# Kernel tuning notes

Measured on AMD Instinct MI355X. Metric: run time of the kernel, lower is better.

## Reference

```python
import jax, jax.numpy as jnp
import numpy as np

LOG2 = float(np.log(2.0))

def _ssp(x):
    # shifted softplus: ln(0.5*(exp(x)+1)) = softplus(x) - ln 2
    return jax.nn.softplus(x) - LOG2

def setup_inputs() -> dict:
    key = jax.random.key(0)
    ks = jax.random.split(key, 8)
    B, N, D = 32, 512, 1024
    H = D // 2
    s = lambda fan_in: 1.0 / np.sqrt(fan_in)
    return {
        "representation": jax.random.normal(ks[0], (B, N, D), jnp.float32),
        "R": jax.random.normal(ks[1], (B, N, 3), jnp.float32),
        "atom_mask": jnp.ones((B, N), jnp.float32),
        "W1": jax.random.normal(ks[2], (D, H), jnp.float32) * s(D),
        "b1": jnp.zeros((H,), jnp.float32),
        "W2": jax.random.normal(ks[3], (H, 1), jnp.float32) * s(H),
        "b2": jnp.zeros((1,), jnp.float32),
        "Wc1": jax.random.normal(ks[4], (D, H), jnp.float32) * s(D),
        "bc1": jnp.zeros((H,), jnp.float32),
        "Wc2": jax.random.normal(ks[5], (H, 1), jnp.float32) * s(H),
        "bc2": jnp.zeros((1,), jnp.float32),
    }

def reference(representation, R, atom_mask, W1, b1, W2, b2, Wc1, bc1, Wc2, bc2):
    B, N, _ = representation.shape
    # Atomwise pyramidal MLP: n_in -> n_in//2 (shifted softplus) -> 1
    yi = _ssp(jnp.einsum("bnd,dh->bnh", representation, W1) + b1)
    yi = jnp.einsum("bnh,ho->bno", yi, W2) + b2            # [B,N,1]
    # masked sum pool over atoms (mean=0, stddev=1 so standardize is identity)
    y = jnp.sum(yi * atom_mask[..., None], axis=1)          # [B,1]

    # pairwise distances with safe sqrt (diag is exactly zero)
    diff = R[:, None, :, :] - R[:, :, None, :]              # [B,N,N,3]
    d2 = jnp.sum(diff * diff, axis=-1)                      # [B,N,N]
    dist = jnp.where(d2 > 0, jnp.sqrt(jnp.where(d2 > 0, d2, 1.0)), 0.0)

    eye = jnp.eye(N, dtype=dist.dtype)
    tot_mask = atom_mask[:, None, :] * atom_mask[:, :, None] * (1.0 - eye)
    keep = (tot_mask != 0).astype(dist.dtype)               # [B,N,N]
    dist = dist * keep

    # charge net: Dense(n_in, n_in//2, ssp) -> Dense(n_in//2, 1)
    q = _ssp(jnp.einsum("bnd,dh->bnh", representation, Wc1) + bc1)
    q = jnp.einsum("bnh,ho->bno", q, Wc2) + bc2             # [B,N,1]

    inv2 = (1e-5 + dist) ** -2                              # [B,N,N]
    coulomb = q[:, :, 0][:, None, :] * inv2 * q             # [B,N,N] (q_j * inv * q_i)
    coulomb = coulomb * keep
    e = jnp.sum(coulomb, axis=(1, 2))                       # [B]

    return y + e[:, None]                                   # [B,1]
```

## Files before the change

kernel.cpp:

```cpp
#include <hip/hip_runtime.h>
#include <math.h>


typedef unsigned short u16;
typedef unsigned int u32;
typedef __bf16 bf16x8 __attribute__((ext_vector_type(8)));
typedef float f32x4 __attribute__((ext_vector_type(4)));

#define GK 1024

#define GLOAD_LDS16(g, l) __builtin_amdgcn_global_load_lds( \
    (const __attribute__((address_space(1))) void*)(g),     \
    (__attribute__((address_space(3))) void*)(l), 16, 0, 0)

__device__ __forceinline__ u16 f2bf(float f) {
    u32 u = __float_as_uint(f);
    return (u16)((u + 0x7FFFu + ((u >> 16) & 1u)) >> 16);
}

__device__ __forceinline__ float ssp_f(float x) {
    return __logf(0.5f * (__expf(x) + 1.0f));
}

__device__ __forceinline__ float ssp_slow(float x) {
    return fmaxf(x, 0.0f) + log1pf(expf(-fabsf(x))) - 0.6931471805599453f;
}


__global__ __launch_bounds__(256) void conv_a(const float* __restrict__ in,
                                              u16* __restrict__ out) {
    int i = (blockIdx.x * 256 + threadIdx.x) * 8;
    float4 x = *(const float4*)(in + i);
    float4 y = *(const float4*)(in + i + 4);
    union { u16 h[8]; uint4 v; } o;
    o.h[0] = f2bf(x.x); o.h[1] = f2bf(x.y); o.h[2] = f2bf(x.z); o.h[3] = f2bf(x.w);
    o.h[4] = f2bf(y.x); o.h[5] = f2bf(y.y); o.h[6] = f2bf(y.z); o.h[7] = f2bf(y.w);
    *(uint4*)(out + i) = o.v;
}

__global__ __launch_bounds__(256) void conv_w(const float* __restrict__ W1,
                                              const float* __restrict__ Wc1,
                                              u16* __restrict__ Bt) {
    __shared__ float tile[32][33];
    const int k0 = blockIdx.x * 32;
    const int n0 = blockIdx.y * 32;
    const float* src = (n0 < 512) ? W1 : Wc1;
    const int ns0 = (n0 < 512) ? n0 : n0 - 512;
    const int t = threadIdx.x;
#pragma unroll
    for (int j = 0; j < 4; j++) {
        int idx = j * 256 + t;
        int kl = idx >> 5, nl = idx & 31;
        tile[kl][nl] = src[(size_t)(k0 + kl) * 512 + ns0 + nl];
    }
    __syncthreads();
#pragma unroll
    for (int j = 0; j < 4; j++) {
        int idx = j * 256 + t;
        int nl = idx >> 5, kl = idx & 31;
        Bt[(size_t)(n0 + nl) * 1024 + k0 + kl] = f2bf(tile[kl][nl]);
    }
}


__global__ __launch_bounds__(256) void gemm_mfma(
    const u16* __restrict__ A,
    const u16* __restrict__ Bt,
    const float* __restrict__ b1, const float* __restrict__ W2,
    const float* __restrict__ bc1, const float* __restrict__ Wc2,
    float* __restrict__ yi_part, float* __restrict__ q_part)
{
    __shared__ u16 As[128 * 32];
    __shared__ u16 Bs[128 * 32];
    const int bm = blockIdx.x;
    const int bn = blockIdx.y;
    const int tid = threadIdx.x;
    const int w = tid >> 6, lane = tid & 63;
    const int wave_m = w & 1, wave_n = w >> 1;
    const int lm = lane & 15, q = lane >> 4;

    f32x4 acc[4][4];
#pragma unroll
    for (int i = 0; i < 4; i++)
#pragma unroll
        for (int j = 0; j < 4; j++)
            acc[i][j] = (f32x4){0.0f, 0.0f, 0.0f, 0.0f};

    const size_t a_base = (size_t)(bm * 128) * GK;
    const size_t b_base = (size_t)(bn * 128) * GK;

    int goff[2];
#pragma unroll
    for (int p = 0; p < 2; p++) {
        int c = (w * 2 + p) * 64 + lane;
        int row = c >> 2;
        int slot = c & 3;
        int k8 = slot ^ ((row >> 2) & 3);
        goff[p] = row * GK + k8 * 8;
    }

    int aoff[4], boff[4];
#pragma unroll
    for (int i = 0; i < 4; i++) {
        int mrow = wave_m * 64 + i * 16 + lm;
        aoff[i] = mrow * 32 + (q ^ ((mrow >> 2) & 3)) * 8;
        int nrow = wave_n * 64 + i * 16 + lm;
        boff[i] = nrow * 32 + (q ^ ((nrow >> 2) & 3)) * 8;
    }

    for (int kt = 0; kt < GK; kt += 32) {
#pragma unroll
        for (int p = 0; p < 2; p++) {
            GLOAD_LDS16(A + a_base + kt + goff[p], &As[(w * 2 + p) << 9]);
            GLOAD_LDS16(Bt + b_base + kt + goff[p], &Bs[(w * 2 + p) << 9]);
        }
        __syncthreads();
        bf16x8 af[4], bfr[4];
#pragma unroll
        for (int i = 0; i < 4; i++) {
            af[i] = *(const bf16x8*)&As[aoff[i]];
            bfr[i] = *(const bf16x8*)&Bs[boff[i]];
        }
#pragma unroll
        for (int i = 0; i < 4; i++)
#pragma unroll
            for (int j = 0; j < 4; j++)
                acc[i][j] = __builtin_amdgcn_mfma_f32_16x16x32_bf16(af[i], bfr[j],
                                                                    acc[i][j], 0, 0, 0);
        __syncthreads();
    }

    const bool is_q = (bn >= 4);
    const float* bb = is_q ? bc1 : b1;
    const float* vv = is_q ? Wc2 : W2;
    float* target = is_q ? q_part : yi_part;
    const int cb0 = (bn & 3) * 128 + wave_n * 64;
    float bias[4], v[4];
#pragma unroll
    for (int j = 0; j < 4; j++) {
        int c = cb0 + j * 16 + lm;
        bias[j] = bb[c];
        v[j] = vv[c];
    }
    const int rowg0 = bm * 128 + wave_m * 64;
#pragma unroll
    for (int i = 0; i < 4; i++) {
#pragma unroll
        for (int r = 0; r < 4; r++) {
            float s = 0.0f;
#pragma unroll
            for (int j = 0; j < 4; j++)
                s += v[j] * ssp_f(acc[i][j][r] + bias[j]);
            s += __shfl_xor(s, 1);
            s += __shfl_xor(s, 2);
            s += __shfl_xor(s, 4);
            s += __shfl_xor(s, 8);
            if (lm == 0) atomicAdd(&target[rowg0 + i * 16 + q * 4 + r], s);
        }
    }
}


__global__ __launch_bounds__(256) void coulomb_k(
    const float* __restrict__ R, const float* __restrict__ mask,
    const float* __restrict__ yi_part, const float* __restrict__ q_part,
    const float* __restrict__ b2p, const float* __restrict__ bc2p,
    float* __restrict__ out)
{
    const int N = 512;
    const int b = blockIdx.y;
    const int chunk = blockIdx.x;
    __shared__ float Rx[512], Ry[512], Rz[512], QM[512];
    __shared__ float rbuf[4];
    const int tid = threadIdx.x;
    const float bc2 = bc2p[0];
    const float b2 = b2p[0];

    for (int j = tid; j < N; j += 256) {
        float m = mask[b * N + j];
        const float* rp = R + ((size_t)b * N + j) * 3;
        Rx[j] = rp[0];
        Ry[j] = rp[1];
        Rz[j] = rp[2];
        QM[j] = (q_part[b * N + j] + bc2) * m;
    }
    __syncthreads();

    const int i = chunk * 64 + (tid & 63);
    const int js = (tid >> 6) * 128;
    const float xi = Rx[i], yi = Ry[i], zi = Rz[i], qmi = QM[i];
    float e = 0.0f;
    for (int j = js; j < js + 128; j++) {
        float dx = xi - Rx[j];
        float dy = yi - Ry[j];
        float dz = zi - Rz[j];
        float d2 = dx * dx + dy * dy + dz * dz;
        float dist = sqrtf(d2);
        float t = 1e-5f + dist;
        float term = qmi * QM[j] / (t * t);
        e += (j == i) ? 0.0f : term;
    }
    if (tid < 64) {
        int ii = chunk * 64 + tid;
        e += (yi_part[b * N + ii] + b2) * mask[b * N + ii];
    }
    for (int off = 32; off > 0; off >>= 1) e += __shfl_down(e, off, 64);
    if ((tid & 63) == 0) rbuf[tid >> 6] = e;
    __syncthreads();
    if (tid == 0) atomicAdd(&out[b], rbuf[0] + rbuf[1] + rbuf[2] + rbuf[3]);
}


#define BM 128
#define BN 64
#define BK 16

__global__ __launch_bounds__(256) void mlp_gemm(
    const float* __restrict__ A, const float* __restrict__ W1,
    const float* __restrict__ Wc1, const float* __restrict__ b1,
    const float* __restrict__ bc1, const float* __restrict__ W2,
    const float* __restrict__ Wc2, float* __restrict__ yi_part,
    float* __restrict__ q_part)
{
    const int K = 1024;
    const int bm = blockIdx.x;
    const int bn = blockIdx.y;
    const bool is_q = (bn >= 8);
    const float* __restrict__ W = is_q ? Wc1 : W1;
    const int j0 = (bn & 7) * BN;

    __shared__ float As[BK][BM + 4];
    __shared__ float Bs[BK][BN + 4];
    __shared__ float red[BM];

    const int tid = threadIdx.x;
    const int tx = tid & 15;
    const int ty = tid >> 4;

    float acc[8][4];
#pragma unroll
    for (int r = 0; r < 8; r++)
#pragma unroll
        for (int c = 0; c < 4; c++) acc[r][c] = 0.0f;

    const int a_row = tid >> 2;
    const int a_k4 = (tid & 3) * 4;
    const float* Arow0 = A + (size_t)(bm * BM + a_row) * K;
    const float* Arow1 = Arow0 + (size_t)64 * K;
    const int w_k = tid >> 4;
    const int w_j = (tid & 15) * 4;

    for (int kt = 0; kt < K; kt += BK) {
        float4 av0 = *(const float4*)(Arow0 + kt + a_k4);
        float4 av1 = *(const float4*)(Arow1 + kt + a_k4);
        float4 wv = *(const float4*)(W + (size_t)(kt + w_k) * 512 + j0 + w_j);
        __syncthreads();
        As[a_k4 + 0][a_row] = av0.x;
        As[a_k4 + 1][a_row] = av0.y;
        As[a_k4 + 2][a_row] = av0.z;
        As[a_k4 + 3][a_row] = av0.w;
        As[a_k4 + 0][a_row + 64] = av1.x;
        As[a_k4 + 1][a_row + 64] = av1.y;
        As[a_k4 + 2][a_row + 64] = av1.z;
        As[a_k4 + 3][a_row + 64] = av1.w;
        *(float4*)&Bs[w_k][w_j] = wv;
        __syncthreads();
#pragma unroll
        for (int kk = 0; kk < BK; kk++) {
            float4 a0 = *(const float4*)&As[kk][ty * 8];
            float4 a1 = *(const float4*)&As[kk][ty * 8 + 4];
            float4 bv = *(const float4*)&Bs[kk][tx * 4];
            float ar[8] = {a0.x, a0.y, a0.z, a0.w, a1.x, a1.y, a1.z, a1.w};
            float bc[4] = {bv.x, bv.y, bv.z, bv.w};
#pragma unroll
            for (int r = 0; r < 8; r++)
#pragma unroll
                for (int c = 0; c < 4; c++)
                    acc[r][c] = fmaf(ar[r], bc[c], acc[r][c]);
        }
    }

    const float* bb = is_q ? bc1 : b1;
    const float* vv = is_q ? Wc2 : W2;
    float bias[4], v[4];
#pragma unroll
    for (int c = 0; c < 4; c++) {
        bias[c] = bb[j0 + tx * 4 + c];
        v[c] = vv[j0 + tx * 4 + c];
    }
    if (tid < BM) red[tid] = 0.0f;
    __syncthreads();
#pragma unroll
    for (int r = 0; r < 8; r++) {
        float s = 0.0f;
#pragma unroll
        for (int c = 0; c < 4; c++)
            s += v[c] * ssp_slow(acc[r][c] + bias[c]);
        atomicAdd(&red[ty * 8 + r], s);
    }
    __syncthreads();
    float* target = is_q ? q_part : yi_part;
    if (tid < BM) atomicAdd(&target[(size_t)bm * BM + tid], red[tid]);
}


extern "C" void kernel_launch(void* const* d_in, const int* in_sizes, int n_in,
                              void* d_out, int out_size, void* d_ws, size_t ws_size,
                              hipStream_t stream) {
    const float* rep  = (const float*)d_in[0];
    const float* R    = (const float*)d_in[1];
    const float* mask = (const float*)d_in[2];
    const float* W1   = (const float*)d_in[3];
    const float* b1   = (const float*)d_in[4];
    const float* W2   = (const float*)d_in[5];
    const float* b2   = (const float*)d_in[6];
    const float* Wc1  = (const float*)d_in[7];
    const float* bc1  = (const float*)d_in[8];
    const float* Wc2  = (const float*)d_in[9];
    const float* bc2  = (const float*)d_in[10];
    float* out = (float*)d_out;

    const size_t szA = 16384ull * 1024 * 2;
    const size_t szB = 1024ull * 1024 * 2;
    const size_t need = szA + szB + 2 * 16384 * sizeof(float);

    if (ws_size >= need) {
        u16* Abf = (u16*)d_ws;
        u16* Btb = (u16*)((char*)d_ws + szA);
        float* yi_part = (float*)((char*)d_ws + szA + szB);
        float* q_part = yi_part + 16384;

        hipMemsetAsync(yi_part, 0, 2 * 16384 * sizeof(float), stream);
        hipMemsetAsync(d_out, 0, 32 * sizeof(float), stream);

        conv_a<<<8192, 256, 0, stream>>>(rep, Abf);
        conv_w<<<dim3(32, 32), 256, 0, stream>>>(W1, Wc1, Btb);
        gemm_mfma<<<dim3(128, 8), 256, 0, stream>>>(Abf, Btb, b1, W2, bc1, Wc2,
                                                    yi_part, q_part);
        coulomb_k<<<dim3(8, 32), 256, 0, stream>>>(R, mask, yi_part, q_part, b2, bc2, out);
    } else {
        float* yi_part = (float*)d_ws;
        float* q_part = yi_part + 16384;
        hipMemsetAsync(d_ws, 0, 2 * 16384 * sizeof(float), stream);
        hipMemsetAsync(d_out, 0, 32 * sizeof(float), stream);
        mlp_gemm<<<dim3(128, 16), 256, 0, stream>>>(rep, W1, Wc1, b1, bc1, W2, Wc2,
                                                    yi_part, q_part);
        coulomb_k<<<dim3(8, 32), 256, 0, stream>>>(R, mask, yi_part, q_part, b2, bc2, out);
    }
}
```

Measured before the change: 190.9 us.

## Merge conversion kernels, deepen GEMM K-tile, drop memsets and atomics

The two bf16 conversion kernels become one launch. The GEMM K step doubles from 32 to 64, with an 8-way XOR swizzle, and each block reduces its partial sums in shared memory before writing them to a per-column-block buffer with plain stores, so global atomics and both memsets go away. The Coulomb stage becomes one 1024-thread block per molecule that sums the partial buffers and writes the output directly. This cuts launch count and synchronisation, but the Coulomb stage now runs on only 32 blocks, which lowers its parallelism.

```diff
diff --git a/kernel.cpp b/kernel.cpp
--- a/kernel.cpp
+++ b/kernel.cpp
@@ -27,38 +27,41 @@
 }
 
 
-__global__ __launch_bounds__(256) void conv_a(const float* __restrict__ in,
-                                              u16* __restrict__ out) {
-    int i = (blockIdx.x * 256 + threadIdx.x) * 8;
-    float4 x = *(const float4*)(in + i);
-    float4 y = *(const float4*)(in + i + 4);
-    union { u16 h[8]; uint4 v; } o;
-    o.h[0] = f2bf(x.x); o.h[1] = f2bf(x.y); o.h[2] = f2bf(x.z); o.h[3] = f2bf(x.w);
-    o.h[4] = f2bf(y.x); o.h[5] = f2bf(y.y); o.h[6] = f2bf(y.z); o.h[7] = f2bf(y.w);
-    *(uint4*)(out + i) = o.v;
-}
-
-__global__ __launch_bounds__(256) void conv_w(const float* __restrict__ W1,
-                                              const float* __restrict__ Wc1,
-                                              u16* __restrict__ Bt) {
+__global__ __launch_bounds__(256) void prep(
+    const float* __restrict__ rep, const float* __restrict__ W1,
+    const float* __restrict__ Wc1, u16* __restrict__ Abf,
+    u16* __restrict__ Btb)
+{
     __shared__ float tile[32][33];
-    const int k0 = blockIdx.x * 32;
-    const int n0 = blockIdx.y * 32;
-    const float* src = (n0 < 512) ? W1 : Wc1;
-    const int ns0 = (n0 < 512) ? n0 : n0 - 512;
+    const int blk = blockIdx.x;
     const int t = threadIdx.x;
-#pragma unroll
-    for (int j = 0; j < 4; j++) {
-        int idx = j * 256 + t;
-        int kl = idx >> 5, nl = idx & 31;
-        tile[kl][nl] = src[(size_t)(k0 + kl) * 512 + ns0 + nl];
-    }
-    __syncthreads();
-#pragma unroll
-    for (int j = 0; j < 4; j++) {
-        int idx = j * 256 + t;
-        int nl = idx >> 5, kl = idx & 31;
-        Bt[(size_t)(n0 + nl) * 1024 + k0 + kl] = f2bf(tile[kl][nl]);
+    if (blk < 8192) {
+        int i = (blk * 256 + t) * 8;
+        float4 x = *(const float4*)(rep + i);
+        float4 y = *(const float4*)(rep + i + 4);
+        union { u16 h[8]; uint4 v; } o;
+        o.h[0] = f2bf(x.x); o.h[1] = f2bf(x.y); o.h[2] = f2bf(x.z); o.h[3] = f2bf(x.w);
+        o.h[4] = f2bf(y.x); o.h[5] = f2bf(y.y); o.h[6] = f2bf(y.z); o.h[7] = f2bf(y.w);
+        *(uint4*)(Abf + i) = o.v;
+    } else {
+        const int bb = blk - 8192;
+        const int k0 = (bb & 31) * 32;
+        const int n0 = (bb >> 5) * 32;
+        const float* src = (n0 < 512) ? W1 : Wc1;
+        const int ns0 = (n0 < 512) ? n0 : n0 - 512;
+#pragma unroll
+        for (int j = 0; j < 4; j++) {
+            int idx = j * 256 + t;
+            int kl = idx >> 5, nl = idx & 31;
+            tile[kl][nl] = src[(size_t)(k0 + kl) * 512 + ns0 + nl];
+        }
+        __syncthreads();
+#pragma unroll
+        for (int j = 0; j < 4; j++) {
+            int idx = j * 256 + t;
+            int nl = idx >> 5, kl = idx & 31;
+            Btb[(size_t)(n0 + nl) * 1024 + k0 + kl] = f2bf(tile[kl][nl]);
+        }
     }
 }
 
@@ -68,10 +71,11 @@
     const u16* __restrict__ Bt,
     const float* __restrict__ b1, const float* __restrict__ W2,
     const float* __restrict__ bc1, const float* __restrict__ Wc2,
-    float* __restrict__ yi_part, float* __restrict__ q_part)
+    float* __restrict__ parts)
 {
-    __shared__ u16 As[128 * 32];
-    __shared__ u16 Bs[128 * 32];
+    __shared__ u16 As[128 * 64];
+    __shared__ u16 Bs[128 * 64];
+    __shared__ float red[2][128];
     const int bm = blockIdx.x;
     const int bn = blockIdx.y;
     const int tid = threadIdx.x;
@@ -89,51 +93,55 @@
     const size_t a_base = (size_t)(bm * 128) * GK;
     const size_t b_base = (size_t)(bn * 128) * GK;
 
-    int goff[2];
-#pragma unroll
-    for (int p = 0; p < 2; p++) {
-        int c = (w * 2 + p) * 64 + lane;
-        int row = c >> 2;
-        int slot = c & 3;
-        int k8 = slot ^ ((row >> 2) & 3);
+    int goff[4];
+#pragma unroll
+    for (int p = 0; p < 4; p++) {
+        int c = (w * 4 + p) * 64 + lane;
+        int row = c >> 3, slot = c & 7;
+        int k8 = slot ^ (row & 7);
         goff[p] = row * GK + k8 * 8;
     }
 
-    int aoff[4], boff[4];
-#pragma unroll
-    for (int i = 0; i < 4; i++) {
-        int mrow = wave_m * 64 + i * 16 + lm;
-        aoff[i] = mrow * 32 + (q ^ ((mrow >> 2) & 3)) * 8;
-        int nrow = wave_n * 64 + i * 16 + lm;
-        boff[i] = nrow * 32 + (q ^ ((nrow >> 2) & 3)) * 8;
-    }
-
-    for (int kt = 0; kt < GK; kt += 32) {
-#pragma unroll
-        for (int p = 0; p < 2; p++) {
-            GLOAD_LDS16(A + a_base + kt + goff[p], &As[(w * 2 + p) << 9]);
-            GLOAD_LDS16(Bt + b_base + kt + goff[p], &Bs[(w * 2 + p) << 9]);
-        }
+    int aoff[2][4], boff[2][4];
+#pragma unroll
+    for (int kk = 0; kk < 2; kk++)
+#pragma unroll
+        for (int i = 0; i < 4; i++) {
+            int mrow = wave_m * 64 + i * 16 + lm;
+            aoff[kk][i] = mrow * 64 + (((kk * 4 + q) ^ (mrow & 7)) << 3);
+            int nrow = wave_n * 64 + i * 16 + lm;
+            boff[kk][i] = nrow * 64 + (((kk * 4 + q) ^ (nrow & 7)) << 3);
+        }
+
+    for (int kt = 0; kt < GK; kt += 64) {
+#pragma unroll
+        for (int p = 0; p < 4; p++)
+            GLOAD_LDS16(A + a_base + kt + goff[p], &As[(w * 4 + p) << 9]);
+#pragma unroll
+        for (int p = 0; p < 4; p++)
+            GLOAD_LDS16(Bt + b_base + kt + goff[p], &Bs[(w * 4 + p) << 9]);
         __syncthreads();
-        bf16x8 af[4], bfr[4];
-#pragma unroll
-        for (int i = 0; i < 4; i++) {
-            af[i] = *(const bf16x8*)&As[aoff[i]];
-            bfr[i] = *(const bf16x8*)&Bs[boff[i]];
-        }
-#pragma unroll
-        for (int i = 0; i < 4; i++)
+#pragma unroll
+        for (int kk = 0; kk < 2; kk++) {
+            bf16x8 bfr[4];
 #pragma unroll
             for (int j = 0; j < 4; j++)
-                acc[i][j] = __builtin_amdgcn_mfma_f32_16x16x32_bf16(af[i], bfr[j],
-                                                                    acc[i][j], 0, 0, 0);
+                bfr[j] = *(const bf16x8*)&Bs[boff[kk][j]];
+#pragma unroll
+            for (int i = 0; i < 4; i++) {
+                bf16x8 af = *(const bf16x8*)&As[aoff[kk][i]];
+#pragma unroll
+                for (int j = 0; j < 4; j++)
+                    acc[i][j] = __builtin_amdgcn_mfma_f32_16x16x32_bf16(
+                        af, bfr[j], acc[i][j], 0, 0, 0);
+            }
+        }
         __syncthreads();
     }
 
     const bool is_q = (bn >= 4);
     const float* bb = is_q ? bc1 : b1;
     const float* vv = is_q ? Wc2 : W2;
-    float* target = is_q ? q_part : yi_part;
     const int cb0 = (bn & 3) * 128 + wave_n * 64;
     float bias[4], v[4];
 #pragma unroll
@@ -142,7 +150,6 @@
         bias[j] = bb[c];
         v[j] = vv[c];
     }
-    const int rowg0 = bm * 128 + wave_m * 64;
 #pragma unroll
     for (int i = 0; i < 4; i++) {
 #pragma unroll
@@ -155,59 +162,70 @@
             s += __shfl_xor(s, 2);
             s += __shfl_xor(s, 4);
             s += __shfl_xor(s, 8);
-            if (lm == 0) atomicAdd(&target[rowg0 + i * 16 + q * 4 + r], s);
-        }
-    }
-}
-
-
-__global__ __launch_bounds__(256) void coulomb_k(
+            if (lm == 0) red[wave_n][wave_m * 64 + i * 16 + q * 4 + r] = s;
+        }
+    }
+    __syncthreads();
+    if (tid < 128) {
+        float val = red[0][tid] + red[1][tid];
+        parts[(size_t)((is_q ? 4 : 0) + (bn & 3)) * 16384 + bm * 128 + tid] = val;
+    }
+}
+
+
+__global__ __launch_bounds__(1024) void coulomb1(
     const float* __restrict__ R, const float* __restrict__ mask,
-    const float* __restrict__ yi_part, const float* __restrict__ q_part,
-    const float* __restrict__ b2p, const float* __restrict__ bc2p,
-    float* __restrict__ out)
+    const float* __restrict__ parts, const float* __restrict__ b2p,
+    const float* __restrict__ bc2p, float* __restrict__ out)
 {
     const int N = 512;
-    const int b = blockIdx.y;
-    const int chunk = blockIdx.x;
+    const int b = blockIdx.x;
     __shared__ float Rx[512], Ry[512], Rz[512], QM[512];
-    __shared__ float rbuf[4];
+    __shared__ float sbuf[16];
     const int tid = threadIdx.x;
-    const float bc2 = bc2p[0];
-    const float b2 = b2p[0];
-
-    for (int j = tid; j < N; j += 256) {
-        float m = mask[b * N + j];
-        const float* rp = R + ((size_t)b * N + j) * 3;
-        Rx[j] = rp[0];
-        Ry[j] = rp[1];
-        Rz[j] = rp[2];
-        QM[j] = (q_part[b * N + j] + bc2) * m;
-    }
-    __syncthreads();
-
-    const int i = chunk * 64 + (tid & 63);
-    const int js = (tid >> 6) * 128;
-    const float xi = Rx[i], yi = Ry[i], zi = Rz[i], qmi = QM[i];
-    float e = 0.0f;
-    for (int j = js; j < js + 128; j++) {
+
+    float yv = 0.0f;
+    if (tid < N) {
+        int idx = b * N + tid;
+        float m = mask[idx];
+        const float* rp = R + (size_t)idx * 3;
+        Rx[tid] = rp[0];
+        Ry[tid] = rp[1];
+        Rz[tid] = rp[2];
+        float qv = parts[4 * 16384 + idx] + parts[5 * 16384 + idx] +
+                   parts[6 * 16384 + idx] + parts[7 * 16384 + idx] + bc2p[0];
+        QM[tid] = qv * m;
+        float yi = parts[0 * 16384 + idx] + parts[1 * 16384 + idx] +
+                   parts[2 * 16384 + idx] + parts[3 * 16384 + idx] + b2p[0];
+        yv = yi * m;
+    }
+    __syncthreads();
+
+    const int i = tid >> 1;
+    const int js = (tid & 1) * 256;
+    const float xi = Rx[i], yy = Ry[i], zi = Rz[i], qmi = QM[i];
+    float e = yv;
+    for (int j = js; j < js + 256; j++) {
         float dx = xi - Rx[j];
-        float dy = yi - Ry[j];
+        float dy = yy - Ry[j];
         float dz = zi - Rz[j];
         float d2 = dx * dx + dy * dy + dz * dz;
-        float dist = sqrtf(d2);
-        float t = 1e-5f + dist;
+        float t = 1e-5f + sqrtf(d2);
         float term = qmi * QM[j] / (t * t);
         e += (j == i) ? 0.0f : term;
     }
+#pragma unroll
+    for (int off = 1; off < 64; off <<= 1) e += __shfl_xor(e, off);
+    if ((tid & 63) == 0) sbuf[tid >> 6] = e;
+    __syncthreads();
     if (tid < 64) {
-        int ii = chunk * 64 + tid;
-        e += (yi_part[b * N + ii] + b2) * mask[b * N + ii];
-    }
-    for (int off = 32; off > 0; off >>= 1) e += __shfl_down(e, off, 64);
-    if ((tid & 63) == 0) rbuf[tid >> 6] = e;
-    __syncthreads();
-    if (tid == 0) atomicAdd(&out[b], rbuf[0] + rbuf[1] + rbuf[2] + rbuf[3]);
+        float t2 = (tid < 16) ? sbuf[tid] : 0.0f;
+        t2 += __shfl_xor(t2, 1);
+        t2 += __shfl_xor(t2, 2);
+        t2 += __shfl_xor(t2, 4);
+        t2 += __shfl_xor(t2, 8);
+        if (tid == 0) out[b] = t2;
+    }
 }
 
 
@@ -303,6 +321,55 @@
     if (tid < BM) atomicAdd(&target[(size_t)bm * BM + tid], red[tid]);
 }
 
+__global__ __launch_bounds__(256) void coulomb_k(
+    const float* __restrict__ R, const float* __restrict__ mask,
+    const float* __restrict__ yi_part, const float* __restrict__ q_part,
+    const float* __restrict__ b2p, const float* __restrict__ bc2p,
+    float* __restrict__ out)
+{
+    const int N = 512;
+    const int b = blockIdx.y;
+    const int chunk = blockIdx.x;
+    __shared__ float Rx[512], Ry[512], Rz[512], QM[512];
+    __shared__ float rbuf[4];
+    const int tid = threadIdx.x;
+    const float bc2 = bc2p[0];
+    const float b2 = b2p[0];
+
+    for (int j = tid; j < N; j += 256) {
+        float m = mask[b * N + j];
+        const float* rp = R + ((size_t)b * N + j) * 3;
+        Rx[j] = rp[0];
+        Ry[j] = rp[1];
+        Rz[j] = rp[2];
+        QM[j] = (q_part[b * N + j] + bc2) * m;
+    }
+    __syncthreads();
+
+    const int i = chunk * 64 + (tid & 63);
+    const int js = (tid >> 6) * 128;
+    const float xi = Rx[i], yi = Ry[i], zi = Rz[i], qmi = QM[i];
+    float e = 0.0f;
+    for (int j = js; j < js + 128; j++) {
+        float dx = xi - Rx[j];
+        float dy = yi - Ry[j];
+        float dz = zi - Rz[j];
+        float d2 = dx * dx + dy * dy + dz * dz;
+        float dist = sqrtf(d2);
+        float t = 1e-5f + dist;
+        float term = qmi * QM[j] / (t * t);
+        e += (j == i) ? 0.0f : term;
+    }
+    if (tid < 64) {
+        int ii = chunk * 64 + tid;
+        e += (yi_part[b * N + ii] + b2) * mask[b * N + ii];
+    }
+    for (int off = 32; off > 0; off >>= 1) e += __shfl_down(e, off, 64);
+    if ((tid & 63) == 0) rbuf[tid >> 6] = e;
+    __syncthreads();
+    if (tid == 0) atomicAdd(&out[b], rbuf[0] + rbuf[1] + rbuf[2] + rbuf[3]);
+}
+
 
 extern "C" void kernel_launch(void* const* d_in, const int* in_sizes, int n_in,
                               void* d_out, int out_size, void* d_ws, size_t ws_size,
@@ -322,22 +389,17 @@
 
     const size_t szA = 16384ull * 1024 * 2;
     const size_t szB = 1024ull * 1024 * 2;
-    const size_t need = szA + szB + 2 * 16384 * sizeof(float);
+    const size_t szP = 8ull * 16384 * 4;
+    const size_t need = szA + szB + szP;
 
     if (ws_size >= need) {
         u16* Abf = (u16*)d_ws;
         u16* Btb = (u16*)((char*)d_ws + szA);
-        float* yi_part = (float*)((char*)d_ws + szA + szB);
-        float* q_part = yi_part + 16384;
-
-        hipMemsetAsync(yi_part, 0, 2 * 16384 * sizeof(float), stream);
-        hipMemsetAsync(d_out, 0, 32 * sizeof(float), stream);
-
-        conv_a<<<8192, 256, 0, stream>>>(rep, Abf);
-        conv_w<<<dim3(32, 32), 256, 0, stream>>>(W1, Wc1, Btb);
-        gemm_mfma<<<dim3(128, 8), 256, 0, stream>>>(Abf, Btb, b1, W2, bc1, Wc2,
-                                                    yi_part, q_part);
-        coulomb_k<<<dim3(8, 32), 256, 0, stream>>>(R, mask, yi_part, q_part, b2, bc2, out);
+        float* parts = (float*)((char*)d_ws + szA + szB);
+
+        prep<<<8192 + 1024, 256, 0, stream>>>(rep, W1, Wc1, Abf, Btb);
+        gemm_mfma<<<dim3(128, 8), 256, 0, stream>>>(Abf, Btb, b1, W2, bc1, Wc2, parts);
+        coulomb1<<<32, 1024, 0, stream>>>(R, mask, parts, b2, bc2, out);
     } else {
         float* yi_part = (float*)d_ws;
         float* q_part = yi_part + 16384;
```

Measured after the change: 232.8 us. +22.0%, slower.
